# Performance work log

Hardware: AMD Instinct MI355X
Metric: run time of the kernel (lower is better)

The kernel has to match this reference:

```python
import jax, jax.numpy as jnp
import numpy as np
import math
from jax import lax

F_SZ = 128      # feature_size
N_HEADS = 8
DH = F_SZ // N_HEADS
LANE_F = 64     # lane_feature_size
NUM_PREDS = 6
LEN_PRED = 30
B, V, T_PAST, N_LANES = 32, 64, 20, 128
SCALE = 1.0 / math.sqrt(DH)


def _heads(x):
    # [..., F] -> [..., H, dh]
    return x.reshape(*x.shape[:-1], N_HEADS, DH)


def _attn(q, k, v):
    # q: [..., H, Nq, dh], k/v: [..., H, Nk, dh] (broadcast over leading dims)
    s = jnp.einsum('...hqd,...hkd->...hqk', q, k) * SCALE
    p = jax.nn.softmax(s, axis=-1)
    return jnp.einsum('...hqk,...hkd->...hqd', p, v)


def _conv1(w, x):
    # 1x1 Conv2d (no bias): w [O,F], x [B,F,V,T]
    return jnp.einsum('of,bfvt->bovt', w, x)


def _to_tbhvd(x):
    # [B,F,V,T] -> [T,B,H,V,dh]  (matches permute(3,0,2,1).view(...).permute(0,1,3,2,4))
    return _heads(x.transpose(3, 0, 2, 1)).transpose(0, 1, 3, 2, 4)


def setup_inputs() -> dict:
    key = jax.random.key(0)
    ks = jax.random.split(key, 32)
    rn = lambda i, shp: jax.random.normal(ks[i], shp, dtype=jnp.float32)
    w = lambda i, shp: rn(i, shp) * 0.05
    return {
        'inputs': rn(0, (B, 2, V, T_PAST)),
        'lanes': rn(1, (B, N_LANES, LANE_F)),
        'pos': rn(2, (B, V, 2)),
        # Embedding conv (2 -> F, kernel (1,3), pad (0,1))
        'emb_w': w(3, (F_SZ, 2, 1, 3)), 'emb_b': w(4, (F_SZ,)),
        # LaneAttentionPast (Linear weights [out,in], no bias)
        'wq_past': w(5, (F_SZ, F_SZ)), 'wk_lanes_p': w(6, (F_SZ, LANE_F)),
        'wv_lanes_p': w(7, (F_SZ, LANE_F)), 'wc_past': w(8, (F_SZ, F_SZ)),
        # SelfAttentionFut (1x1 convs, no bias)
        'wk_fut': w(9, (F_SZ, F_SZ)), 'wq_fut_sa': w(10, (F_SZ, F_SZ)),
        'wv_fut': w(11, (F_SZ, F_SZ)), 'wc_fut_sa': w(12, (F_SZ, F_SZ)),
        # LaneAttentionFut
        'wk_lanes_f': w(13, (F_SZ, LANE_F)), 'wv_lanes_f': w(14, (F_SZ, LANE_F)),
        'wq_fut_la': w(15, (F_SZ, F_SZ)), 'wc_fut_la': w(16, (F_SZ, F_SZ)),
        # MultiOutputLayer (1x1 convs with bias)
        'w1': w(17, (F_SZ, F_SZ)), 'b1': w(18, (F_SZ,)),
        'w2': w(19, (F_SZ, F_SZ)), 'b2': w(20, (F_SZ,)),
        'wo': w(21, (6 * NUM_PREDS, F_SZ)), 'bo': w(22, (6 * NUM_PREDS,)),
    }


def reference(inputs, lanes, pos, emb_w, emb_b, wq_past, wk_lanes_p, wv_lanes_p,
              wc_past, wk_fut, wq_fut_sa, wv_fut, wc_fut_sa, wk_lanes_f,
              wv_lanes_f, wq_fut_la, wc_fut_la, w1, b1, w2, b2, wo, bo):
    # ---- Embedding: Conv2d(2->F, (1,3), pad (0,1)) over [B,2,V,T_past]
    emb = lax.conv_general_dilated(
        inputs, emb_w, (1, 1), ((0, 0), (1, 1)),
        dimension_numbers=('NCHW', 'OIHW', 'NCHW')) + emb_b[None, :, None, None]
    feat = emb[:, :, :, -1].transpose(0, 2, 1)            # [B,V,F] last timestep

    # ---- LaneAttentionPast: vehicles attend to lanes
    q = _heads(feat @ wq_past.T).transpose(0, 2, 1, 3)    # [B,H,V,dh]
    k = _heads(lanes @ wk_lanes_p.T).transpose(0, 2, 1, 3)  # [B,H,nl,dh]
    v = _heads(lanes @ wv_lanes_p.T).transpose(0, 2, 1, 3)
    o = _attn(q, k, v).transpose(0, 2, 1, 3).reshape(B, V, F_SZ)
    feat = o @ wc_past.T + feat                           # residual

    # ---- tile over prediction horizon: h [B,F,V,T]
    h = jnp.broadcast_to(feat.transpose(0, 2, 1)[:, :, :, None],
                         (B, F_SZ, V, LEN_PRED))

    # ---- SelfAttentionFut: per-timestep vehicle-vehicle attention
    k = _to_tbhvd(_conv1(wk_fut, h))                      # [T,B,H,V,dh]
    q = _to_tbhvd(_conv1(wq_fut_sa, h))
    vv = _to_tbhvd(_conv1(wv_fut, h))
    o = _attn(q, k, vv).transpose(0, 1, 3, 2, 4).reshape(LEN_PRED, B, V, F_SZ)
    h = _conv1(wc_fut_sa, o.transpose(1, 3, 2, 0)) + h    # residual

    # ---- LaneAttentionFut: per-timestep vehicle-lane attention
    kl = _heads(lanes @ wk_lanes_f.T).transpose(0, 2, 1, 3)[None]  # [1,B,H,nl,dh]
    vl = _heads(lanes @ wv_lanes_f.T).transpose(0, 2, 1, 3)[None]
    q = _to_tbhvd(_conv1(wq_fut_la, h))                   # [T,B,H,V,dh]
    o = _attn(q, kl, vl).transpose(0, 1, 3, 2, 4).reshape(LEN_PRED, B, V, F_SZ)
    h = _conv1(wc_fut_la, o.transpose(1, 3, 2, 0)) + h    # residual

    z = jax.nn.relu(_conv1(w1, h) + b1[None, :, None, None])
    z = jax.nn.relu(_conv1(w2, z) + b2[None, :, None, None])
    z = _conv1(wo, z) + bo[None, :, None, None]           # [B,6P,V,T]
    x = z.transpose(3, 0, 2, 1).reshape(LEN_PRED, B, V, NUM_PREDS, 6)

    # ---- outputActivation (Gaussian-mixture params)
    p = jax.nn.softmax(x[..., 5:6] / math.sqrt(NUM_PREDS), axis=3)
    posr = pos.reshape(1, B, V, 1, 2)
    muX = x[..., 0:1] + posr[..., 0:1]
    muY = x[..., 1:2] + posr[..., 1:2]
    sigX = jnp.exp(x[..., 2:3] * 0.5)
    sigY = jnp.exp(x[..., 3:4] * 0.5)
    rho = jnp.tanh(x[..., 4:5])
    return jnp.concatenate([muX, muY, sigX, sigY, rho, p], axis=4)
```

## Files before the change

kernel.cpp:

```cpp
#include <hip/hip_runtime.h>
#include <hip/hip_bf16.h>
#include <math.h>

typedef __hip_bfloat16 bf16;
typedef float4 f4;

#define B 32
#define V 64
#define F 128
#define NL 128
#define H 8
#define DH 16
#define LEN_PRED 30

#define OFF_EMBW 0
#define OFF_EMBB 768
#define OFF_B1   896
#define OFF_B2   1024
#define OFF_BO   1152
#define WCP_T    1216
#define WCSA_T   17600
#define WCLA_T   33984
#define W1_T     50368
#define W2_T     66752
#define WO_T     83136
#define OFF_FEAT1 87744
#define OFF_FEAT2 349888
#define OFF_OSA1  612032
#define OFF_OSA2  874176

struct InPtrs { const void* p[23]; };

__device__ __forceinline__ float dot4(f4 a, f4 b) {
    return a.x * b.x + a.y * b.y + a.z * b.z + a.w * b.w;
}

__device__ __forceinline__ int detect_f32(const void* lanesraw, int t) {
    const unsigned short* u = (const unsigned short*)lanesraw;
    int lane = t & 63;
    int wild = 0;
    for (int j = 0; j < 4; j++) {
        int e = (u[lane * 4 + j] >> 7) & 0xFF;
        if (e != 0 && (e < 90 || e > 164)) wild++;
    }
    unsigned long long m = __ballot(wild > 0);
    return (__popcll(m) >= 16) ? 1 : 0;
}

__device__ __forceinline__ float ldin(const void* p, int i, int fl) {
    return fl ? ((const float*)p)[i] : __bfloat162float(((const bf16*)p)[i]);
}

__device__ void phase_prep(float* sm, const InPtrs& ptrs, int fl, float* ws, int seg) {
    const int srci[11] = {3, 4, 18, 20, 22, 8, 12, 16, 17, 19, 21};
    const int szs[11]  = {768, 128, 128, 128, 36, 16384, 16384, 16384, 16384, 16384, 4608};
    const int dsto[11] = {OFF_EMBW, OFF_EMBB, OFF_B1, OFF_B2, OFF_BO,
                          WCP_T, WCSA_T, WCLA_T, W1_T, W2_T, WO_T};
    const int Otab[11] = {0, 0, 0, 0, 0, 128, 128, 128, 128, 128, 36};
    int t = threadIdx.x;
    int n = szs[seg], O = Otab[seg];
    const void* src = ptrs.p[srci[seg]];
    if (O == 0) {
        for (int i = t; i < n; i += 512) ws[dsto[seg] + i] = ldin(src, i, fl);
        return;
    }
    float* tile = sm;
    for (int i = t; i < n; i += 512) {
        int o = i >> 7, k = i & 127;
        tile[o * 129 + k] = ldin(src, i, fl);
    }
    __syncthreads();
    float* dst = ws + dsto[seg];
    for (int j = t; j < n; j += 512) {
        int k = j / O, o = j - k * O;
        dst[j] = tile[o * 129 + k];
    }
}

__device__ void phase_attn_lane_past(float* sm, const InPtrs& ptrs,
                                     int b, int h, int fl, float* osa) {
    int t = threadIdx.x;
    float* ln   = sm;
    float* xs   = sm + 8704;
    float* wql  = sm + 17152;
    float* wkl  = sm + 19264;
    float* wvl  = sm + 20352;
    float* kh   = sm + 21440;
    float* vhT  = sm + 24000;
    float* qh   = sm + 26112;
    float* rsum = sm + 27392;
    float* in4  = sm + 27456;
    float* s    = ln;

    int lb = b * NL * 64;
    for (int i = t; i < NL * 64; i += 512)
        ln[(i >> 6) * 68 + (i & 63)] = ldin(ptrs.p[1], lb + i, fl);
    for (int i = t; i < 2048; i += 512)
        wql[(i >> 7) * 132 + (i & 127)] = ldin(ptrs.p[5], h * 2048 + i, fl);
    for (int i = t; i < 1024; i += 512)
        wkl[(i >> 6) * 68 + (i & 63)] = ldin(ptrs.p[6], h * 1024 + i, fl);
    for (int i = t; i < 1024; i += 512)
        wvl[(i >> 6) * 68 + (i & 63)] = ldin(ptrs.p[7], h * 1024 + i, fl);
    if (t < 64) {
        in4[t * 4 + 0] = ldin(ptrs.p[0], ((b * 2 + 0) * 64 + t) * 20 + 18, fl);
        in4[t * 4 + 1] = ldin(ptrs.p[0], ((b * 2 + 0) * 64 + t) * 20 + 19, fl);
        in4[t * 4 + 2] = ldin(ptrs.p[0], ((b * 2 + 1) * 64 + t) * 20 + 18, fl);
        in4[t * 4 + 3] = ldin(ptrs.p[0], ((b * 2 + 1) * 64 + t) * 20 + 19, fl);
    }
    __syncthreads();
    for (int i = t; i < 8192; i += 512) {
        int v = i >> 7, c = i & 127;
        xs[v * 132 + c] = ldin(ptrs.p[4], c, fl)
            + in4[v * 4 + 0] * ldin(ptrs.p[3], c * 6 + 0, fl)
            + in4[v * 4 + 1] * ldin(ptrs.p[3], c * 6 + 1, fl)
            + in4[v * 4 + 2] * ldin(ptrs.p[3], c * 6 + 3, fl)
            + in4[v * 4 + 3] * ldin(ptrs.p[3], c * 6 + 4, fl);
    }
    __syncthreads();

    if (t < 256) {
        int l0 = t >> 3, d0 = (t & 7) * 2;
        float ak[4][2] = {}, av[4][2] = {};
        for (int kk = 0; kk < 64; kk += 4) {
            f4 L[4], WK[2], WV[2];
            #pragma unroll
            for (int m = 0; m < 4; m++) L[m] = *(const f4*)&ln[(l0 + 32 * m) * 68 + kk];
            #pragma unroll
            for (int j = 0; j < 2; j++) {
                WK[j] = *(const f4*)&wkl[(d0 + j) * 68 + kk];
                WV[j] = *(const f4*)&wvl[(d0 + j) * 68 + kk];
            }
            #pragma unroll
            for (int m = 0; m < 4; m++)
                #pragma unroll
                for (int j = 0; j < 2; j++) {
                    ak[m][j] += dot4(L[m], WK[j]);
                    av[m][j] += dot4(L[m], WV[j]);
                }
        }
        #pragma unroll
        for (int m = 0; m < 4; m++)
            #pragma unroll
            for (int j = 0; j < 2; j++) {
                int l = l0 + 32 * m, d = d0 + j;
                kh[l * 20 + d] = ak[m][j];
                vhT[d * 132 + l] = av[m][j];
            }
    } else {
        int tt = t - 256, v = tt >> 2, d0 = (tt & 3) * 4;
        float aq[4] = {};
        for (int kk = 0; kk < 128; kk += 4) {
            f4 X = *(const f4*)&xs[v * 132 + kk];
            #pragma unroll
            for (int i2 = 0; i2 < 4; i2++)
                aq[i2] += dot4(X, *(const f4*)&wql[(d0 + i2) * 132 + kk]);
        }
        #pragma unroll
        for (int i2 = 0; i2 < 4; i2++) qh[v * 20 + d0 + i2] = aq[i2];
    }
    __syncthreads();

    {
        int v0 = t >> 5, l0 = t & 31;
        float sc[4][4] = {};
        #pragma unroll
        for (int kd = 0; kd < 16; kd += 4) {
            f4 Q[4], K4[4];
            #pragma unroll
            for (int m = 0; m < 4; m++) Q[m] = *(const f4*)&qh[(v0 + 16 * m) * 20 + kd];
            #pragma unroll
            for (int i2 = 0; i2 < 4; i2++) K4[i2] = *(const f4*)&kh[(l0 + 32 * i2) * 20 + kd];
            #pragma unroll
            for (int m = 0; m < 4; m++)
                #pragma unroll
                for (int i2 = 0; i2 < 4; i2++) sc[m][i2] += dot4(Q[m], K4[i2]);
        }
        #pragma unroll
        for (int m = 0; m < 4; m++)
            #pragma unroll
            for (int i2 = 0; i2 < 4; i2++)
                s[(v0 + 16 * m) * 132 + l0 + 32 * i2] = sc[m][i2] * 0.25f;
    }
    __syncthreads();

    {
        int v = t >> 3, j = t & 7;
        float* sr = s + v * 132;
        float m = -1e30f;
        for (int k = j; k < NL; k += 8) m = fmaxf(m, sr[k]);
        for (int off = 1; off < 8; off <<= 1) m = fmaxf(m, __shfl_xor(m, off));
        float sum = 0.f;
        for (int k = j; k < NL; k += 8) { float e = __expf(sr[k] - m); sr[k] = e; sum += e; }
        for (int off = 1; off < 8; off <<= 1) sum += __shfl_xor(sum, off);
        if (j == 0) rsum[v] = sum;
    }
    __syncthreads();

    if (t < 256) {
        int v = t >> 2, d0 = (t & 3) * 4;
        float o4[4] = {};
        for (int ll = 0; ll < NL; ll += 4) {
            f4 S4 = *(const f4*)&s[v * 132 + ll];
            #pragma unroll
            for (int i2 = 0; i2 < 4; i2++)
                o4[i2] += dot4(S4, *(const f4*)&vhT[(d0 + i2) * 132 + ll]);
        }
        float* ob = osa + b * 8192 + h * 16;
        float inv = 1.0f / rsum[v];
        #pragma unroll
        for (int i2 = 0; i2 < 4; i2++) ob[v * F + d0 + i2] = o4[i2] * inv;
    }
}

__global__ __launch_bounds__(512) void k1_lap(InPtrs ptrs, float* __restrict__ ws) {
    int bid = blockIdx.x, b = bid >> 3, h = bid & 7, t = threadIdx.x;
    int fl = detect_f32(ptrs.p[1], t);
    __shared__ __align__(16) float sm[27712];
    phase_attn_lane_past(sm, ptrs, b, h, fl, ws + OFF_OSA1);
    __syncthreads();
    if (bid >= 245) phase_prep(sm, ptrs, fl, ws, bid - 245);
}

__global__ __launch_bounds__(512) void k2_saf(InPtrs ptrs, float* __restrict__ ws) {
    int bid = blockIdx.x, b = bid >> 3, h = bid & 7, t = threadIdx.x;
    int fl = detect_f32(ptrs.p[1], t);
    __shared__ __align__(16) float smem[23488];
    float* osap = smem;
    float* qh   = smem;
    float* kh   = smem + 1280;
    float* vhT  = smem + 2560;
    float* s2   = smem + 3648;
    float* rsum = smem + 8000;
    float* xs   = smem + 8448;
    float* wsl  = smem + 16896;
    float* in4  = smem + 23232;

    const float* o1 = ws + OFF_OSA1 + b * 8192;
    for (int i = t; i < 8192; i += 512) osap[(i >> 7) * 132 + (i & 127)] = o1[i];
    for (int i = t; i < 2048; i += 512) {
        int r = i >> 7, c = i & 127;
        wsl[r * 132 + c]        = ldin(ptrs.p[10], h * 2048 + i, fl);
        wsl[2112 + r * 132 + c] = ldin(ptrs.p[9],  h * 2048 + i, fl);
        wsl[4224 + r * 132 + c] = ldin(ptrs.p[11], h * 2048 + i, fl);
    }
    if (t < 64) {
        in4[t * 4 + 0] = ldin(ptrs.p[0], ((b * 2 + 0) * 64 + t) * 20 + 18, fl);
        in4[t * 4 + 1] = ldin(ptrs.p[0], ((b * 2 + 0) * 64 + t) * 20 + 19, fl);
        in4[t * 4 + 2] = ldin(ptrs.p[0], ((b * 2 + 1) * 64 + t) * 20 + 18, fl);
        in4[t * 4 + 3] = ldin(ptrs.p[0], ((b * 2 + 1) * 64 + t) * 20 + 19, fl);
    }
    __syncthreads();
    for (int i = t; i < 8192; i += 512) {
        int v = i >> 7, c = i & 127;
        xs[v * 132 + c] = ldin(ptrs.p[4], c, fl)
            + in4[v * 4 + 0] * ldin(ptrs.p[3], c * 6 + 0, fl)
            + in4[v * 4 + 1] * ldin(ptrs.p[3], c * 6 + 1, fl)
            + in4[v * 4 + 2] * ldin(ptrs.p[3], c * 6 + 3, fl)
            + in4[v * 4 + 3] * ldin(ptrs.p[3], c * 6 + 4, fl);
    }
    __syncthreads();
    {
        const float* wT = ws + WCP_T;
        int v0 = (t >> 5) * 4, c0 = (t & 31) * 4;
        float acc[4][4];
        #pragma unroll
        for (int m = 0; m < 4; m++) {
            f4 X0 = *(const f4*)&xs[(v0 + m) * 132 + c0];
            acc[m][0] = X0.x; acc[m][1] = X0.y; acc[m][2] = X0.z; acc[m][3] = X0.w;
        }
        for (int k = 0; k < 128; k += 4) {
            f4 W0 = *(const f4*)&wT[(k + 0) * 128 + c0];
            f4 W1 = *(const f4*)&wT[(k + 1) * 128 + c0];
            f4 W2 = *(const f4*)&wT[(k + 2) * 128 + c0];
            f4 W3 = *(const f4*)&wT[(k + 3) * 128 + c0];
            #pragma unroll
            for (int m = 0; m < 4; m++) {
                f4 X = *(const f4*)&osap[(v0 + m) * 132 + k];
                acc[m][0] += X.x * W0.x + X.y * W1.x + X.z * W2.x + X.w * W3.x;
                acc[m][1] += X.x * W0.y + X.y * W1.y + X.z * W2.y + X.w * W3.y;
                acc[m][2] += X.x * W0.z + X.y * W1.z + X.z * W2.z + X.w * W3.z;
                acc[m][3] += X.x * W0.w + X.y * W1.w + X.z * W2.w + X.w * W3.w;
            }
        }
        #pragma unroll
        for (int m = 0; m < 4; m++)
            *(f4*)&xs[(v0 + m) * 132 + c0] =
                make_float4(acc[m][0], acc[m][1], acc[m][2], acc[m][3]);
    }
    __syncthreads();
    if (h == 0) {
        float* f1 = ws + OFF_FEAT1 + b * 8192;
        for (int i = t; i < 8192; i += 512) f1[i] = xs[(i >> 7) * 132 + (i & 127)];
    }
    __syncthreads();

    if (t < 256) {
        int v = t >> 2, d0 = (t & 3) * 4;
        float aq[4] = {};
        for (int kk = 0; kk < 128; kk += 4) {
            f4 X = *(const f4*)&xs[v * 132 + kk];
            #pragma unroll
            for (int i2 = 0; i2 < 4; i2++)
                aq[i2] += dot4(X, *(const f4*)&wsl[(d0 + i2) * 132 + kk]);
        }
        #pragma unroll
        for (int i2 = 0; i2 < 4; i2++) qh[v * 20 + d0 + i2] = aq[i2];
    } else if (t < 384) {
        int tt = t - 256, v = tt >> 1, d0 = (tt & 1) * 8;
        float ak[8] = {};
        for (int kk = 0; kk < 128; kk += 4) {
            f4 X = *(const f4*)&xs[v * 132 + kk];
            #pragma unroll
            for (int i2 = 0; i2 < 8; i2++)
                ak[i2] += dot4(X, *(const f4*)&wsl[2112 + (d0 + i2) * 132 + kk]);
        }
        #pragma unroll
        for (int i2 = 0; i2 < 8; i2++) kh[v * 20 + d0 + i2] = ak[i2];
    } else {
        int tt = t - 384, v = tt >> 1, d0 = (tt & 1) * 8;
        float av[8] = {};
        for (int kk = 0; kk < 128; kk += 4) {
            f4 X = *(const f4*)&xs[v * 132 + kk];
            #pragma unroll
            for (int i2 = 0; i2 < 8; i2++)
                av[i2] += dot4(X, *(const f4*)&wsl[4224 + (d0 + i2) * 132 + kk]);
        }
        #pragma unroll
        for (int i2 = 0; i2 < 8; i2++) vhT[(d0 + i2) * 68 + v] = av[i2];
    }
    __syncthreads();

    {
        int v0 = t >> 5, l0 = t & 31;
        float sc[4][2] = {};
        #pragma unroll
        for (int kd = 0; kd < 16; kd += 4) {
            f4 Q[4], K2[2];
            #pragma unroll
            for (int m = 0; m < 4; m++) Q[m] = *(const f4*)&qh[(v0 + 16 * m) * 20 + kd];
            #pragma unroll
            for (int i2 = 0; i2 < 2; i2++) K2[i2] = *(const f4*)&kh[(l0 + 32 * i2) * 20 + kd];
            #pragma unroll
            for (int m = 0; m < 4; m++)
                #pragma unroll
                for (int i2 = 0; i2 < 2; i2++) sc[m][i2] += dot4(Q[m], K2[i2]);
        }
        #pragma unroll
        for (int m = 0; m < 4; m++)
            #pragma unroll
            for (int i2 = 0; i2 < 2; i2++)
                s2[(v0 + 16 * m) * 68 + l0 + 32 * i2] = sc[m][i2] * 0.25f;
    }
    __syncthreads();

    {
        int v = t >> 3, j = t & 7;
        float* sr = s2 + v * 68;
        float m = -1e30f;
        for (int k = j; k < V; k += 8) m = fmaxf(m, sr[k]);
        for (int off = 1; off < 8; off <<= 1) m = fmaxf(m, __shfl_xor(m, off));
        float sum = 0.f;
        for (int k = j; k < V; k += 8) { float e = __expf(sr[k] - m); sr[k] = e; sum += e; }
        for (int off = 1; off < 8; off <<= 1) sum += __shfl_xor(sum, off);
        if (j == 0) rsum[v] = sum;
    }
    __syncthreads();

    if (t < 256) {
        int v = t >> 2, d0 = (t & 3) * 4;
        float o4[4] = {};
        for (int ll = 0; ll < V; ll += 4) {
            f4 S4 = *(const f4*)&s2[v * 68 + ll];
            #pragma unroll
            for (int i2 = 0; i2 < 4; i2++)
                o4[i2] += dot4(S4, *(const f4*)&vhT[(d0 + i2) * 68 + ll]);
        }
        float* ob = ws + OFF_OSA2 + b * 8192 + h * 16;
        float inv = 1.0f / rsum[v];
        #pragma unroll
        for (int i2 = 0; i2 < 4; i2++) ob[v * F + d0 + i2] = o4[i2] * inv;
    }
}

__global__ __launch_bounds__(512) void k3_laf(InPtrs ptrs, float* __restrict__ ws) {
    int bid = blockIdx.x, b = bid >> 3, h = bid & 7, t = threadIdx.x;
    int fl = detect_f32(ptrs.p[1], t);
    __shared__ __align__(16) float smem[29888];
    float* ln   = smem;
    float* osas = smem + 8704;
    float* kh   = smem + 8704;
    float* vhT  = smem + 11264;
    float* qh   = smem + 13376;
    float* rsum = smem + 14656;
    float* xs   = smem + 17152;
    float* wql  = smem + 25600;
    float* wkl  = smem + 27712;
    float* wvl  = smem + 28800;
    float* s    = ln;

    int lb = b * NL * 64;
    for (int i = t; i < NL * 64; i += 512)
        ln[(i >> 6) * 68 + (i & 63)] = ldin(ptrs.p[1], lb + i, fl);
    const float* o2 = ws + OFF_OSA2 + b * 8192;
    for (int i = t; i < 8192; i += 512) osas[(i >> 7) * 132 + (i & 127)] = o2[i];
    for (int i = t; i < 2048; i += 512)
        wql[(i >> 7) * 132 + (i & 127)] = ldin(ptrs.p[15], h * 2048 + i, fl);
    for (int i = t; i < 1024; i += 512)
        wkl[(i >> 6) * 68 + (i & 63)] = ldin(ptrs.p[13], h * 1024 + i, fl);
    for (int i = t; i < 1024; i += 512)
        wvl[(i >> 6) * 68 + (i & 63)] = ldin(ptrs.p[14], h * 1024 + i, fl);
    __syncthreads();
    {
        const float* wT = ws + WCSA_T;
        const float* f1 = ws + OFF_FEAT1 + b * 8192;
        int v0 = (t >> 5) * 4, c0 = (t & 31) * 4;
        float acc[4][4];
        #pragma unroll
        for (int m = 0; m < 4; m++) {
            f4 X0 = *(const f4*)&f1[(v0 + m) * 128 + c0];
            acc[m][0] = X0.x; acc[m][1] = X0.y; acc[m][2] = X0.z; acc[m][3] = X0.w;
        }
        for (int k = 0; k < 128; k += 4) {
            f4 W0 = *(const f4*)&wT[(k + 0) * 128 + c0];
            f4 W1 = *(const f4*)&wT[(k + 1) * 128 + c0];
            f4 W2 = *(const f4*)&wT[(k + 2) * 128 + c0];
            f4 W3 = *(const f4*)&wT[(k + 3) * 128 + c0];
            #pragma unroll
            for (int m = 0; m < 4; m++) {
                f4 X = *(const f4*)&osas[(v0 + m) * 132 + k];
                acc[m][0] += X.x * W0.x + X.y * W1.x + X.z * W2.x + X.w * W3.x;
                acc[m][1] += X.x * W0.y + X.y * W1.y + X.z * W2.y + X.w * W3.y;
                acc[m][2] += X.x * W0.z + X.y * W1.z + X.z * W2.z + X.w * W3.z;
                acc[m][3] += X.x * W0.w + X.y * W1.w + X.z * W2.w + X.w * W3.w;
            }
        }
        #pragma unroll
        for (int m = 0; m < 4; m++)
            *(f4*)&xs[(v0 + m) * 132 + c0] =
                make_float4(acc[m][0], acc[m][1], acc[m][2], acc[m][3]);
    }
    __syncthreads();
    if (h == 0) {
        float* f2 = ws + OFF_FEAT2 + b * 8192;
        for (int i = t; i < 8192; i += 512) f2[i] = xs[(i >> 7) * 132 + (i & 127)];
    }
    __syncthreads();

    if (t < 256) {
        int l0 = t >> 3, d0 = (t & 7) * 2;
        float ak[4][2] = {}, av[4][2] = {};
        for (int kk = 0; kk < 64; kk += 4) {
            f4 L[4], WK[2], WV[2];
            #pragma unroll
            for (int m = 0; m < 4; m++) L[m] = *(const f4*)&ln[(l0 + 32 * m) * 68 + kk];
            #pragma unroll
            for (int j = 0; j < 2; j++) {
                WK[j] = *(const f4*)&wkl[(d0 + j) * 68 + kk];
                WV[j] = *(const f4*)&wvl[(d0 + j) * 68 + kk];
            }
            #pragma unroll
            for (int m = 0; m < 4; m++)
                #pragma unroll
                for (int j = 0; j < 2; j++) {
                    ak[m][j] += dot4(L[m], WK[j]);
                    av[m][j] += dot4(L[m], WV[j]);
                }
        }
        #pragma unroll
        for (int m = 0; m < 4; m++)
            #pragma unroll
            for (int j = 0; j < 2; j++) {
                int l = l0 + 32 * m, d = d0 + j;
                kh[l * 20 + d] = ak[m][j];
                vhT[d * 132 + l] = av[m][j];
            }
    } else {
        int tt = t - 256, v = tt >> 2, d0 = (tt & 3) * 4;
        float aq[4] = {};
        for (int kk = 0; kk < 128; kk += 4) {
            f4 X = *(const f4*)&xs[v * 132 + kk];
            #pragma unroll
            for (int i2 = 0; i2 < 4; i2++)
                aq[i2] += dot4(X, *(const f4*)&wql[(d0 + i2) * 132 + kk]);
        }
        #pragma unroll
        for (int i2 = 0; i2 < 4; i2++) qh[v * 20 + d0 + i2] = aq[i2];
    }
    __syncthreads();

    {
        int v0 = t >> 5, l0 = t & 31;
        float sc[4][4] = {};
        #pragma unroll
        for (int kd = 0; kd < 16; kd += 4) {
            f4 Q[4], K4[4];
            #pragma unroll
            for (int m = 0; m < 4; m++) Q[m] = *(const f4*)&qh[(v0 + 16 * m) * 20 + kd];
            #pragma unroll
            for (int i2 = 0; i2 < 4; i2++) K4[i2] = *(const f4*)&kh[(l0 + 32 * i2) * 20 + kd];
            #pragma unroll
            for (int m = 0; m < 4; m++)
                #pragma unroll
                for (int i2 = 0; i2 < 4; i2++) sc[m][i2] += dot4(Q[m], K4[i2]);
        }
        #pragma unroll
        for (int m = 0; m < 4; m++)
            #pragma unroll
            for (int i2 = 0; i2 < 4; i2++)
                s[(v0 + 16 * m) * 132 + l0 + 32 * i2] = sc[m][i2] * 0.25f;
    }
    __syncthreads();

    {
        int v = t >> 3, j = t & 7;
        float* sr = s + v * 132;
        float m = -1e30f;
        for (int k = j; k < NL; k += 8) m = fmaxf(m, sr[k]);
        for (int off = 1; off < 8; off <<= 1) m = fmaxf(m, __shfl_xor(m, off));
        float sum = 0.f;
        for (int k = j; k < NL; k += 8) { float e = __expf(sr[k] - m); sr[k] = e; sum += e; }
        for (int off = 1; off < 8; off <<= 1) sum += __shfl_xor(sum, off);
        if (j == 0) rsum[v] = sum;
    }
    __syncthreads();

    if (t < 256) {
        int v = t >> 2, d0 = (t & 3) * 4;
        float o4[4] = {};
        for (int ll = 0; ll < NL; ll += 4) {
            f4 S4 = *(const f4*)&s[v * 132 + ll];
            #pragma unroll
            for (int i2 = 0; i2 < 4; i2++)
                o4[i2] += dot4(S4, *(const f4*)&vhT[(d0 + i2) * 132 + ll]);
        }
        float* ob = ws + OFF_OSA1 + b * 8192 + h * 16;
        float inv = 1.0f / rsum[v];
        #pragma unroll
        for (int i2 = 0; i2 < 4; i2++) ob[v * F + d0 + i2] = o4[i2] * inv;
    }
}

__global__ __launch_bounds__(512) void k4_out(InPtrs ptrs, float* __restrict__ ws,
                                              void* __restrict__ out) {
    int bid = blockIdx.x, t = threadIdx.x;
    int fl = detect_f32(ptrs.p[1], t);
    __shared__ float sm[4416];
    const float* ola  = ws + OFF_OSA1;
    const float* feat = ws + OFF_FEAT2;
    int bvl = t >> 6, tt = t & 63;
    int bv = bid * 8 + bvl;
    float* orow = sm + bvl * 128;
    float* h3   = sm + 1024 + bvl * 128;
    float* z1   = sm + 2048 + bvl * 128;
    float* z2   = sm + 3072 + bvl * 128;
    float* z3all = sm + 4096;
    float* z3   = z3all + bvl * 40;
    orow[tt] = ola[bv * 128 + tt];
    orow[tt + 64] = ola[bv * 128 + tt + 64];
    __syncthreads();
    const float* wclaT = ws + WCLA_T;
    float a0 = 0.f, a1 = 0.f;
    for (int k = 0; k < 128; k++) {
        float x = orow[k];
        a0 += x * wclaT[k * 128 + tt]; a1 += x * wclaT[k * 128 + tt + 64];
    }
    h3[tt] = a0 + feat[bv * 128 + tt];
    h3[tt + 64] = a1 + feat[bv * 128 + tt + 64];
    __syncthreads();
    const float* w1T = ws + W1_T;
    a0 = ws[OFF_B1 + tt]; a1 = ws[OFF_B1 + tt + 64];
    for (int k = 0; k < 128; k++) {
        float x = h3[k];
        a0 += x * w1T[k * 128 + tt]; a1 += x * w1T[k * 128 + tt + 64];
    }
    z1[tt] = fmaxf(a0, 0.f); z1[tt + 64] = fmaxf(a1, 0.f);
    __syncthreads();
    const float* w2T = ws + W2_T;
    a0 = ws[OFF_B2 + tt]; a1 = ws[OFF_B2 + tt + 64];
    for (int k = 0; k < 128; k++) {
        float x = z1[k];
        a0 += x * w2T[k * 128 + tt]; a1 += x * w2T[k * 128 + tt + 64];
    }
    z2[tt] = fmaxf(a0, 0.f); z2[tt + 64] = fmaxf(a1, 0.f);
    __syncthreads();
    const float* woT = ws + WO_T;
    if (tt < 36) {
        float a = ws[OFF_BO + tt];
        for (int k = 0; k < 128; k++) a += z2[k] * woT[k * 36 + tt];
        z3[tt] = a;
    }
    __syncthreads();
    float r = 0.f;
    if (tt < 36) {
        int c = tt % 6;
        float xv = z3[tt];
        if (c == 0)      r = xv + ldin(ptrs.p[2], bv * 2 + 0, fl);
        else if (c == 1) r = xv + ldin(ptrs.p[2], bv * 2 + 1, fl);
        else if (c == 2 || c == 3) r = __expf(0.5f * xv);
        else if (c == 4) r = tanhf(xv);
        else {
            const float inv = 0.4082482904638631f;
            float m = -1e30f;
            for (int pp = 0; pp < 6; pp++) m = fmaxf(m, z3[pp * 6 + 5] * inv);
            float sum = 0.f;
            for (int pp = 0; pp < 6; pp++) sum += __expf(z3[pp * 6 + 5] * inv - m);
            r = __expf(xv * inv - m) / sum;
        }
    }
    __syncthreads();
    if (tt < 36) z3[tt] = r;
    __syncthreads();
    int base = bid * 288;
    if (fl) {
        float* o = (float*)out;
        for (int i = t; i < LEN_PRED * 288; i += 512) {
            int ttp = i / 288, idx = i - ttp * 288;
            o[ttp * 73728 + base + idx] = z3all[(idx / 36) * 40 + idx % 36];
        }
    } else {
        bf16* o = (bf16*)out;
        for (int i = t; i < LEN_PRED * 288; i += 512) {
            int ttp = i / 288, idx = i - ttp * 288;
            o[ttp * 73728 + base + idx] = __float2bfloat16(z3all[(idx / 36) * 40 + idx % 36]);
        }
    }
}

extern "C" void kernel_launch(void* const* d_in, const int* in_sizes, int n_in,
                              void* d_out, int out_size, void* d_ws, size_t ws_size,
                              hipStream_t stream) {
    float* ws = (float*)d_ws;
    InPtrs ptrs;
    for (int i = 0; i < 23; i++) ptrs.p[i] = d_in[i];
    k1_lap<<<256, 512, 0, stream>>>(ptrs, ws);
    k2_saf<<<256, 512, 0, stream>>>(ptrs, ws);
    k3_laf<<<256, 512, 0, stream>>>(ptrs, ws);
    k4_out<<<256, 512, 0, stream>>>(ptrs, ws, d_out);
}
```

Before: 125.1 us.

## Spread weight conversion across all blocks and vectorize loads with untransposed weights

Replaces the tail-block weight transpose/prep phase in k1 with a grid-strided, untransposed fp32 conversion spread over all blocks. The pos input is also converted into the workspace. Input and weight staging loads are vectorized to float4 with an inline bf16 unpack. The matmuls in k2, k3 and k4 are rewritten to read row-major weights as float4 dot products along k. The goal is to remove the serialized tail work of a few blocks and cut scalar global loads. In exchange, k4 now does per-thread strided row reads of the weights, which are less coalesced.

After: 168.3 us. 34.5% more time.

```diff
diff --git a/kernel.cpp b/kernel.cpp
--- a/kernel.cpp
+++ b/kernel.cpp
@@ -13,21 +13,22 @@
 #define DH 16
 #define LEN_PRED 30
 
-#define OFF_EMBW 0
-#define OFF_EMBB 768
-#define OFF_B1   896
-#define OFF_B2   1024
-#define OFF_BO   1152
-#define WCP_T    1216
-#define WCSA_T   17600
-#define WCLA_T   33984
-#define W1_T     50368
-#define W2_T     66752
-#define WO_T     83136
-#define OFF_FEAT1 87744
-#define OFF_FEAT2 349888
-#define OFF_OSA1  612032
-#define OFF_OSA2  874176
+#define WEMBW 0
+#define WEMBB 768
+#define WB1   896
+#define WB2   1024
+#define WBO   1152
+#define WPOS  1192
+#define WWCP  5288
+#define WWCSA 21672
+#define WWCLA 38056
+#define WW1   54440
+#define WW2   70824
+#define WWO   87208
+#define OFF_FEAT1 91904
+#define OFF_FEAT2 354048
+#define OFF_OSA1  616192
+#define OFF_OSA2  878336
 
 struct InPtrs { const void* p[23]; };
 
@@ -51,35 +52,36 @@
     return fl ? ((const float*)p)[i] : __bfloat162float(((const bf16*)p)[i]);
 }
 
-__device__ void phase_prep(float* sm, const InPtrs& ptrs, int fl, float* ws, int seg) {
-    const int srci[11] = {3, 4, 18, 20, 22, 8, 12, 16, 17, 19, 21};
-    const int szs[11]  = {768, 128, 128, 128, 36, 16384, 16384, 16384, 16384, 16384, 4608};
-    const int dsto[11] = {OFF_EMBW, OFF_EMBB, OFF_B1, OFF_B2, OFF_BO,
-                          WCP_T, WCSA_T, WCLA_T, W1_T, W2_T, WO_T};
-    const int Otab[11] = {0, 0, 0, 0, 0, 128, 128, 128, 128, 128, 36};
-    int t = threadIdx.x;
-    int n = szs[seg], O = Otab[seg];
-    const void* src = ptrs.p[srci[seg]];
-    if (O == 0) {
-        for (int i = t; i < n; i += 512) ws[dsto[seg] + i] = ldin(src, i, fl);
-        return;
-    }
-    float* tile = sm;
-    for (int i = t; i < n; i += 512) {
-        int o = i >> 7, k = i & 127;
-        tile[o * 129 + k] = ldin(src, i, fl);
-    }
-    __syncthreads();
-    float* dst = ws + dsto[seg];
-    for (int j = t; j < n; j += 512) {
-        int k = j / O, o = j - k * O;
-        dst[j] = tile[o * 129 + k];
-    }
-}
-
-__device__ void phase_attn_lane_past(float* sm, const InPtrs& ptrs,
-                                     int b, int h, int fl, float* osa) {
-    int t = threadIdx.x;
+__device__ __forceinline__ f4 ldin4(const void* p, int i, int fl) {
+    if (fl) return *(const f4*)((const float*)p + i);
+    ushort4 v = *(const ushort4*)((const unsigned short*)p + i);
+    f4 r;
+    r.x = __uint_as_float((unsigned)v.x << 16);
+    r.y = __uint_as_float((unsigned)v.y << 16);
+    r.z = __uint_as_float((unsigned)v.z << 16);
+    r.w = __uint_as_float((unsigned)v.w << 16);
+    return r;
+}
+
+__device__ void convert_weights(const InPtrs& ptrs, int fl, float* ws, int bid) {
+    const int srci[12] = {3, 4, 18, 20, 22, 2, 8, 12, 16, 17, 19, 21};
+    const int szs[12]  = {768, 128, 128, 128, 36, 4096,
+                          16384, 16384, 16384, 16384, 16384, 4608};
+    const int dsto[12] = {WEMBW, WEMBB, WB1, WB2, WBO, WPOS,
+                          WWCP, WWCSA, WWCLA, WW1, WW2, WWO};
+    int gidx = bid * 512 + threadIdx.x;
+    #pragma unroll
+    for (int s = 0; s < 12; s++) {
+        const void* src = ptrs.p[srci[s]];
+        float* dst = ws + dsto[s];
+        for (int i = gidx; i < szs[s]; i += 131072) dst[i] = ldin(src, i, fl);
+    }
+}
+
+__global__ __launch_bounds__(512) void k1_lap(InPtrs ptrs, float* __restrict__ ws) {
+    int bid = blockIdx.x, b = bid >> 3, h = bid & 7, t = threadIdx.x;
+    int fl = detect_f32(ptrs.p[1], t);
+    __shared__ __align__(16) float sm[27712];
     float* ln   = sm;
     float* xs   = sm + 8704;
     float* wql  = sm + 17152;
@@ -91,21 +93,34 @@
     float* rsum = sm + 27392;
     float* in4  = sm + 27456;
     float* s    = ln;
-
-    int lb = b * NL * 64;
-    for (int i = t; i < NL * 64; i += 512)
-        ln[(i >> 6) * 68 + (i & 63)] = ldin(ptrs.p[1], lb + i, fl);
-    for (int i = t; i < 2048; i += 512)
-        wql[(i >> 7) * 132 + (i & 127)] = ldin(ptrs.p[5], h * 2048 + i, fl);
-    for (int i = t; i < 1024; i += 512)
-        wkl[(i >> 6) * 68 + (i & 63)] = ldin(ptrs.p[6], h * 1024 + i, fl);
-    for (int i = t; i < 1024; i += 512)
-        wvl[(i >> 6) * 68 + (i & 63)] = ldin(ptrs.p[7], h * 1024 + i, fl);
-    if (t < 64) {
-        in4[t * 4 + 0] = ldin(ptrs.p[0], ((b * 2 + 0) * 64 + t) * 20 + 18, fl);
-        in4[t * 4 + 1] = ldin(ptrs.p[0], ((b * 2 + 0) * 64 + t) * 20 + 19, fl);
-        in4[t * 4 + 2] = ldin(ptrs.p[0], ((b * 2 + 1) * 64 + t) * 20 + 18, fl);
-        in4[t * 4 + 3] = ldin(ptrs.p[0], ((b * 2 + 1) * 64 + t) * 20 + 19, fl);
+    float* osa  = ws + OFF_OSA1;
+
+    convert_weights(ptrs, fl, ws, bid);
+
+    {
+        int lb = b * NL * 64;
+        for (int i = t * 4; i < NL * 64; i += 2048) {
+            f4 w = ldin4(ptrs.p[1], lb + i, fl);
+            *(f4*)&ln[(i >> 6) * 68 + (i & 63)] = w;
+        }
+        {
+            int i = t * 4;
+            f4 w = ldin4(ptrs.p[5], h * 2048 + i, fl);
+            *(f4*)&wql[(i >> 7) * 132 + (i & 127)] = w;
+        }
+        if (t < 256) {
+            int i = t * 4;
+            f4 w = ldin4(ptrs.p[6], h * 1024 + i, fl);
+            *(f4*)&wkl[(i >> 6) * 68 + (i & 63)] = w;
+            w = ldin4(ptrs.p[7], h * 1024 + i, fl);
+            *(f4*)&wvl[(i >> 6) * 68 + (i & 63)] = w;
+        }
+        if (t < 64) {
+            in4[t * 4 + 0] = ldin(ptrs.p[0], ((b * 2 + 0) * 64 + t) * 20 + 18, fl);
+            in4[t * 4 + 1] = ldin(ptrs.p[0], ((b * 2 + 0) * 64 + t) * 20 + 19, fl);
+            in4[t * 4 + 2] = ldin(ptrs.p[0], ((b * 2 + 1) * 64 + t) * 20 + 18, fl);
+            in4[t * 4 + 3] = ldin(ptrs.p[0], ((b * 2 + 1) * 64 + t) * 20 + 19, fl);
+        }
     }
     __syncthreads();
     for (int i = t; i < 8192; i += 512) {
@@ -210,15 +225,6 @@
         #pragma unroll
         for (int i2 = 0; i2 < 4; i2++) ob[v * F + d0 + i2] = o4[i2] * inv;
     }
-}
-
-__global__ __launch_bounds__(512) void k1_lap(InPtrs ptrs, float* __restrict__ ws) {
-    int bid = blockIdx.x, b = bid >> 3, h = bid & 7, t = threadIdx.x;
-    int fl = detect_f32(ptrs.p[1], t);
-    __shared__ __align__(16) float sm[27712];
-    phase_attn_lane_past(sm, ptrs, b, h, fl, ws + OFF_OSA1);
-    __syncthreads();
-    if (bid >= 245) phase_prep(sm, ptrs, fl, ws, bid - 245);
 }
 
 __global__ __launch_bounds__(512) void k2_saf(InPtrs ptrs, float* __restrict__ ws) {
@@ -236,12 +242,16 @@
     float* in4  = smem + 23232;
 
     const float* o1 = ws + OFF_OSA1 + b * 8192;
-    for (int i = t; i < 8192; i += 512) osap[(i >> 7) * 132 + (i & 127)] = o1[i];
-    for (int i = t; i < 2048; i += 512) {
-        int r = i >> 7, c = i & 127;
-        wsl[r * 132 + c]        = ldin(ptrs.p[10], h * 2048 + i, fl);
-        wsl[2112 + r * 132 + c] = ldin(ptrs.p[9],  h * 2048 + i, fl);
-        wsl[4224 + r * 132 + c] = ldin(ptrs.p[11], h * 2048 + i, fl);
+    for (int i = t * 4; i < 8192; i += 2048)
+        *(f4*)&osap[(i >> 7) * 132 + (i & 127)] = *(const f4*)&o1[i];
+    {
+        int i = t * 4;
+        f4 w = ldin4(ptrs.p[10], h * 2048 + i, fl);
+        *(f4*)&wsl[(i >> 7) * 132 + (i & 127)] = w;
+        w = ldin4(ptrs.p[9], h * 2048 + i, fl);
+        *(f4*)&wsl[2112 + (i >> 7) * 132 + (i & 127)] = w;
+        w = ldin4(ptrs.p[11], h * 2048 + i, fl);
+        *(f4*)&wsl[4224 + (i >> 7) * 132 + (i & 127)] = w;
     }
     if (t < 64) {
         in4[t * 4 + 0] = ldin(ptrs.p[0], ((b * 2 + 0) * 64 + t) * 20 + 18, fl);
@@ -252,15 +262,15 @@
     __syncthreads();
     for (int i = t; i < 8192; i += 512) {
         int v = i >> 7, c = i & 127;
-        xs[v * 132 + c] = ldin(ptrs.p[4], c, fl)
-            + in4[v * 4 + 0] * ldin(ptrs.p[3], c * 6 + 0, fl)
-            + in4[v * 4 + 1] * ldin(ptrs.p[3], c * 6 + 1, fl)
-            + in4[v * 4 + 2] * ldin(ptrs.p[3], c * 6 + 3, fl)
-            + in4[v * 4 + 3] * ldin(ptrs.p[3], c * 6 + 4, fl);
-    }
-    __syncthreads();
-    {
-        const float* wT = ws + WCP_T;
+        xs[v * 132 + c] = ws[WEMBB + c]
+            + in4[v * 4 + 0] * ws[WEMBW + c * 6 + 0]
+            + in4[v * 4 + 1] * ws[WEMBW + c * 6 + 1]
+            + in4[v * 4 + 2] * ws[WEMBW + c * 6 + 3]
+            + in4[v * 4 + 3] * ws[WEMBW + c * 6 + 4];
+    }
+    __syncthreads();
+    {
+        const float* wcp = ws + WWCP;
         int v0 = (t >> 5) * 4, c0 = (t & 31) * 4;
         float acc[4][4];
         #pragma unroll
@@ -268,19 +278,16 @@
             f4 X0 = *(const f4*)&xs[(v0 + m) * 132 + c0];
             acc[m][0] = X0.x; acc[m][1] = X0.y; acc[m][2] = X0.z; acc[m][3] = X0.w;
         }
-        for (int k = 0; k < 128; k += 4) {
-            f4 W0 = *(const f4*)&wT[(k + 0) * 128 + c0];
-            f4 W1 = *(const f4*)&wT[(k + 1) * 128 + c0];
-            f4 W2 = *(const f4*)&wT[(k + 2) * 128 + c0];
-            f4 W3 = *(const f4*)&wT[(k + 3) * 128 + c0];
-            #pragma unroll
-            for (int m = 0; m < 4; m++) {
-                f4 X = *(const f4*)&osap[(v0 + m) * 132 + k];
-                acc[m][0] += X.x * W0.x + X.y * W1.x + X.z * W2.x + X.w * W3.x;
-                acc[m][1] += X.x * W0.y + X.y * W1.y + X.z * W2.y + X.w * W3.y;
-                acc[m][2] += X.x * W0.z + X.y * W1.z + X.z * W2.z + X.w * W3.z;
-                acc[m][3] += X.x * W0.w + X.y * W1.w + X.z * W2.w + X.w * W3.w;
-            }
+        for (int kk = 0; kk < 128; kk += 4) {
+            f4 X[4], W[4];
+            #pragma unroll
+            for (int m = 0; m < 4; m++) X[m] = *(const f4*)&osap[(v0 + m) * 132 + kk];
+            #pragma unroll
+            for (int j = 0; j < 4; j++) W[j] = *(const f4*)&wcp[(c0 + j) * 128 + kk];
+            #pragma unroll
+            for (int m = 0; m < 4; m++)
+                #pragma unroll
+                for (int j = 0; j < 4; j++) acc[m][j] += dot4(X[m], W[j]);
         }
         #pragma unroll
         for (int m = 0; m < 4; m++)
@@ -398,20 +405,31 @@
     float* wvl  = smem + 28800;
     float* s    = ln;
 
-    int lb = b * NL * 64;
-    for (int i = t; i < NL * 64; i += 512)
-        ln[(i >> 6) * 68 + (i & 63)] = ldin(ptrs.p[1], lb + i, fl);
-    const float* o2 = ws + OFF_OSA2 + b * 8192;
-    for (int i = t; i < 8192; i += 512) osas[(i >> 7) * 132 + (i & 127)] = o2[i];
-    for (int i = t; i < 2048; i += 512)
-        wql[(i >> 7) * 132 + (i & 127)] = ldin(ptrs.p[15], h * 2048 + i, fl);
-    for (int i = t; i < 1024; i += 512)
-        wkl[(i >> 6) * 68 + (i & 63)] = ldin(ptrs.p[13], h * 1024 + i, fl);
-    for (int i = t; i < 1024; i += 512)
-        wvl[(i >> 6) * 68 + (i & 63)] = ldin(ptrs.p[14], h * 1024 + i, fl);
-    __syncthreads();
-    {
-        const float* wT = ws + WCSA_T;
+    {
+        int lb = b * NL * 64;
+        for (int i = t * 4; i < NL * 64; i += 2048) {
+            f4 w = ldin4(ptrs.p[1], lb + i, fl);
+            *(f4*)&ln[(i >> 6) * 68 + (i & 63)] = w;
+        }
+        const float* o2 = ws + OFF_OSA2 + b * 8192;
+        for (int i = t * 4; i < 8192; i += 2048)
+            *(f4*)&osas[(i >> 7) * 132 + (i & 127)] = *(const f4*)&o2[i];
+        {
+            int i = t * 4;
+            f4 w = ldin4(ptrs.p[15], h * 2048 + i, fl);
+            *(f4*)&wql[(i >> 7) * 132 + (i & 127)] = w;
+        }
+        if (t < 256) {
+            int i = t * 4;
+            f4 w = ldin4(ptrs.p[13], h * 1024 + i, fl);
+            *(f4*)&wkl[(i >> 6) * 68 + (i & 63)] = w;
+            w = ldin4(ptrs.p[14], h * 1024 + i, fl);
+            *(f4*)&wvl[(i >> 6) * 68 + (i & 63)] = w;
+        }
+    }
+    __syncthreads();
+    {
+        const float* wcsa = ws + WWCSA;
         const float* f1 = ws + OFF_FEAT1 + b * 8192;
         int v0 = (t >> 5) * 4, c0 = (t & 31) * 4;
         float acc[4][4];
@@ -420,19 +438,16 @@
             f4 X0 = *(const f4*)&f1[(v0 + m) * 128 + c0];
             acc[m][0] = X0.x; acc[m][1] = X0.y; acc[m][2] = X0.z; acc[m][3] = X0.w;
         }
-        for (int k = 0; k < 128; k += 4) {
-            f4 W0 = *(const f4*)&wT[(k + 0) * 128 + c0];
-            f4 W1 = *(const f4*)&wT[(k + 1) * 128 + c0];
-            f4 W2 = *(const f4*)&wT[(k + 2) * 128 + c0];
-            f4 W3 = *(const f4*)&wT[(k + 3) * 128 + c0];
-            #pragma unroll
-            for (int m = 0; m < 4; m++) {
-                f4 X = *(const f4*)&osas[(v0 + m) * 132 + k];
-                acc[m][0] += X.x * W0.x + X.y * W1.x + X.z * W2.x + X.w * W3.x;
-                acc[m][1] += X.x * W0.y + X.y * W1.y + X.z * W2.y + X.w * W3.y;
-                acc[m][2] += X.x * W0.z + X.y * W1.z + X.z * W2.z + X.w * W3.z;
-                acc[m][3] += X.x * W0.w + X.y * W1.w + X.z * W2.w + X.w * W3.w;
-            }
+        for (int kk = 0; kk < 128; kk += 4) {
+            f4 X[4], W[4];
+            #pragma unroll
+            for (int m = 0; m < 4; m++) X[m] = *(const f4*)&osas[(v0 + m) * 132 + kk];
+            #pragma unroll
+            for (int j = 0; j < 4; j++) W[j] = *(const f4*)&wcsa[(c0 + j) * 128 + kk];
+            #pragma unroll
+            for (int m = 0; m < 4; m++)
+                #pragma unroll
+                for (int j = 0; j < 4; j++) acc[m][j] += dot4(X[m], W[j]);
         }
         #pragma unroll
         for (int m = 0; m < 4; m++)
@@ -544,10 +559,10 @@
                                               void* __restrict__ out) {
     int bid = blockIdx.x, t = threadIdx.x;
     int fl = detect_f32(ptrs.p[1], t);
-    __shared__ float sm[4416];
+    __shared__ __align__(16) float sm[4416];
     const float* ola  = ws + OFF_OSA1;
     const float* feat = ws + OFF_FEAT2;
-    int bvl = t >> 6, tt = t & 63;
+    int bvl = t >> 6, u = t & 63;
     int bv = bid * 8 + bvl;
     float* orow = sm + bvl * 128;
     float* h3   = sm + 1024 + bvl * 128;
@@ -555,47 +570,62 @@
     float* z2   = sm + 3072 + bvl * 128;
     float* z3all = sm + 4096;
     float* z3   = z3all + bvl * 40;
-    orow[tt] = ola[bv * 128 + tt];
-    orow[tt + 64] = ola[bv * 128 + tt + 64];
-    __syncthreads();
-    const float* wclaT = ws + WCLA_T;
-    float a0 = 0.f, a1 = 0.f;
-    for (int k = 0; k < 128; k++) {
-        float x = orow[k];
-        a0 += x * wclaT[k * 128 + tt]; a1 += x * wclaT[k * 128 + tt + 64];
-    }
-    h3[tt] = a0 + feat[bv * 128 + tt];
-    h3[tt + 64] = a1 + feat[bv * 128 + tt + 64];
-    __syncthreads();
-    const float* w1T = ws + W1_T;
-    a0 = ws[OFF_B1 + tt]; a1 = ws[OFF_B1 + tt + 64];
-    for (int k = 0; k < 128; k++) {
-        float x = h3[k];
-        a0 += x * w1T[k * 128 + tt]; a1 += x * w1T[k * 128 + tt + 64];
-    }
-    z1[tt] = fmaxf(a0, 0.f); z1[tt + 64] = fmaxf(a1, 0.f);
-    __syncthreads();
-    const float* w2T = ws + W2_T;
-    a0 = ws[OFF_B2 + tt]; a1 = ws[OFF_B2 + tt + 64];
-    for (int k = 0; k < 128; k++) {
-        float x = z1[k];
-        a0 += x * w2T[k * 128 + tt]; a1 += x * w2T[k * 128 + tt + 64];
-    }
-    z2[tt] = fmaxf(a0, 0.f); z2[tt + 64] = fmaxf(a1, 0.f);
-    __syncthreads();
-    const float* woT = ws + WO_T;
-    if (tt < 36) {
-        float a = ws[OFF_BO + tt];
-        for (int k = 0; k < 128; k++) a += z2[k] * woT[k * 36 + tt];
-        z3[tt] = a;
+    orow[u] = ola[bv * 128 + u];
+    orow[u + 64] = ola[bv * 128 + u + 64];
+    __syncthreads();
+    {
+        const float* w = ws + WWCLA;
+        int c0 = u * 2;
+        float a0 = 0.f, a1 = 0.f;
+        for (int kk = 0; kk < 128; kk += 4) {
+            f4 X = *(const f4*)&orow[kk];
+            a0 += dot4(X, *(const f4*)&w[(c0 + 0) * 128 + kk]);
+            a1 += dot4(X, *(const f4*)&w[(c0 + 1) * 128 + kk]);
+        }
+        h3[c0]     = a0 + feat[bv * 128 + c0];
+        h3[c0 + 1] = a1 + feat[bv * 128 + c0 + 1];
+    }
+    __syncthreads();
+    {
+        const float* w = ws + WW1;
+        int c0 = u * 2;
+        float a0 = ws[WB1 + c0], a1 = ws[WB1 + c0 + 1];
+        for (int kk = 0; kk < 128; kk += 4) {
+            f4 X = *(const f4*)&h3[kk];
+            a0 += dot4(X, *(const f4*)&w[(c0 + 0) * 128 + kk]);
+            a1 += dot4(X, *(const f4*)&w[(c0 + 1) * 128 + kk]);
+        }
+        z1[c0] = fmaxf(a0, 0.f); z1[c0 + 1] = fmaxf(a1, 0.f);
+    }
+    __syncthreads();
+    {
+        const float* w = ws + WW2;
+        int c0 = u * 2;
+        float a0 = ws[WB2 + c0], a1 = ws[WB2 + c0 + 1];
+        for (int kk = 0; kk < 128; kk += 4) {
+            f4 X = *(const f4*)&z1[kk];
+            a0 += dot4(X, *(const f4*)&w[(c0 + 0) * 128 + kk]);
+            a1 += dot4(X, *(const f4*)&w[(c0 + 1) * 128 + kk]);
+        }
+        z2[c0] = fmaxf(a0, 0.f); z2[c0 + 1] = fmaxf(a1, 0.f);
+    }
+    __syncthreads();
+    if (u < 36) {
+        const float* w = ws + WWO;
+        float a = ws[WBO + u];
+        for (int kk = 0; kk < 128; kk += 4) {
+            f4 X = *(const f4*)&z2[kk];
+            a += dot4(X, *(const f4*)&w[u * 128 + kk]);
+        }
+        z3[u] = a;
     }
     __syncthreads();
     float r = 0.f;
-    if (tt < 36) {
-        int c = tt % 6;
-        float xv = z3[tt];
-        if (c == 0)      r = xv + ldin(ptrs.p[2], bv * 2 + 0, fl);
-        else if (c == 1) r = xv + ldin(ptrs.p[2], bv * 2 + 1, fl);
+    if (u < 36) {
+        int c = u % 6;
+        float xv = z3[u];
+        if (c == 0)      r = xv + ws[WPOS + bv * 2 + 0];
+        else if (c == 1) r = xv + ws[WPOS + bv * 2 + 1];
         else if (c == 2 || c == 3) r = __expf(0.5f * xv);
         else if (c == 4) r = tanhf(xv);
         else {
@@ -608,7 +638,7 @@
         }
     }
     __syncthreads();
-    if (tt < 36) z3[tt] = r;
+    if (u < 36) z3[u] = r;
     __syncthreads();
     int base = bid * 288;
     if (fl) {
```
